# Kernel optimization log

Measured on AMD Instinct MI355X. Metric: run time of the kernel, lower is better.

The kernel has to match this reference:

```python
import jax, jax.numpy as jnp
import numpy as np

N = 50000      # nodes
E = 600000     # edges
D_IN = 128
D_HID = 128
D_OUT = 64
BN_EPS = 1e-5


def _linear(key, fan_in, fan_out):
    s = 1.0 / np.sqrt(fan_in)
    kw, kb = jax.random.split(key)
    W = jax.random.uniform(kw, (fan_in, fan_out), jnp.float32, -s, s)
    b = jax.random.uniform(kb, (fan_out,), jnp.float32, -s, s)
    return W, b


def setup_inputs() -> dict:
    key = jax.random.key(0)
    ks = jax.random.split(key, 6)
    x = jax.random.normal(ks[0], (N, D_IN), jnp.float32)
    edge_index = jax.random.randint(ks[1], (2, E), 0, N, dtype=jnp.int64)
    W1, b1 = _linear(ks[2], D_IN, D_HID)
    W2, b2 = _linear(ks[3], D_HID, D_HID)
    W3, b3 = _linear(ks[4], D_HID, D_OUT)
    g1 = jnp.ones((D_HID,), jnp.float32); be1 = jnp.zeros((D_HID,), jnp.float32)
    g2 = jnp.ones((D_HID,), jnp.float32); be2 = jnp.zeros((D_HID,), jnp.float32)
    return {"x": x, "edge_index": edge_index,
            "W1": W1, "b1": b1, "g1": g1, "be1": be1,
            "W2": W2, "b2": b2, "g2": g2, "be2": be2,
            "W3": W3, "b3": b3}


def _gin_conv(x, src, dst, W, b):
    # GIN aggregation: h_i = (1+eps)*x_i + sum_{j->i} x_j, eps=0, then linear
    agg = jax.ops.segment_sum(x[src], dst, num_segments=N)  # [N, d]
    return (agg + x) @ W + b


def _bn(x, gamma, beta):
    # BatchNorm1d in training mode: batch statistics over nodes
    m = x.mean(axis=0)
    v = x.var(axis=0)
    return (x - m) * jax.lax.rsqrt(v + BN_EPS) * gamma + beta


def reference(x, edge_index, W1, b1, g1, be1, W2, b2, g2, be2, W3, b3):
    src, dst = edge_index[0], edge_index[1]
    h = jax.nn.relu(_bn(_gin_conv(x, src, dst, W1, b1), g1, be1))
    h = jax.nn.relu(_bn(_gin_conv(h, src, dst, W2, b2), g2, be2))
    h = _gin_conv(h, src, dst, W3, b3)
    return jax.nn.log_softmax(h, axis=-1)
```

## Files before the change

kernel.cpp:

```cpp
#include <hip/hip_runtime.h>

#define BN_EPS 1e-5f

typedef __attribute__((ext_vector_type(8))) __bf16 bf16x8;
typedef __attribute__((ext_vector_type(4))) float f32x4;

__device__ __forceinline__ unsigned short f2bf(float f) {
    unsigned int u = __float_as_uint(f);
    u = (u + 0x7fffu + ((u >> 16) & 1u)) >> 16;
    return (unsigned short)u;
}
__device__ __forceinline__ float bfLo(unsigned int w) { return __uint_as_float(w << 16); }
__device__ __forceinline__ float bfHi(unsigned int w) { return __uint_as_float(w & 0xffff0000u); }

__device__ __forceinline__ void accRow(float* acc, uint4 v) {
    acc[0] += bfLo(v.x); acc[1] += bfHi(v.x);
    acc[2] += bfLo(v.y); acc[3] += bfHi(v.y);
    acc[4] += bfLo(v.z); acc[5] += bfHi(v.z);
    acc[6] += bfLo(v.w); acc[7] += bfHi(v.w);
}
__device__ __forceinline__ void accRowBN(float* acc, uint4 v, const float* a8, const float* c8) {
    acc[0] += fmaxf(fmaf(bfLo(v.x), a8[0], c8[0]), 0.f);
    acc[1] += fmaxf(fmaf(bfHi(v.x), a8[1], c8[1]), 0.f);
    acc[2] += fmaxf(fmaf(bfLo(v.y), a8[2], c8[2]), 0.f);
    acc[3] += fmaxf(fmaf(bfHi(v.y), a8[3], c8[3]), 0.f);
    acc[4] += fmaxf(fmaf(bfLo(v.z), a8[4], c8[4]), 0.f);
    acc[5] += fmaxf(fmaf(bfHi(v.z), a8[5], c8[5]), 0.f);
    acc[6] += fmaxf(fmaf(bfLo(v.w), a8[6], c8[6]), 0.f);
    acc[7] += fmaxf(fmaf(bfHi(v.w), a8[7], c8[7]), 0.f);
}


__global__ void hist_kernel(const int* __restrict__ dst, int* __restrict__ deg, int E) {
    int e = blockIdx.x * blockDim.x + threadIdx.x;
    if (e < E) atomicAdd(&deg[dst[e]], 1);
}

__global__ void scan_block(const int* __restrict__ deg, int* __restrict__ incl,
                           int* __restrict__ bsum, int N) {
    __shared__ int s[256];
    int i = blockIdx.x * 256 + threadIdx.x;
    int v = (i < N) ? deg[i] : 0;
    s[threadIdx.x] = v;
    __syncthreads();
#pragma unroll
    for (int off = 1; off < 256; off <<= 1) {
        int t = (threadIdx.x >= off) ? s[threadIdx.x - off] : 0;
        __syncthreads();
        s[threadIdx.x] += t;
        __syncthreads();
    }
    if (i < N) incl[i] = s[threadIdx.x];
    if (threadIdx.x == 255) bsum[blockIdx.x] = s[255];
}

__global__ void scan_top(int* __restrict__ bsum, int nb) {
    __shared__ int s[256];
    int v = (threadIdx.x < nb) ? bsum[threadIdx.x] : 0;
    s[threadIdx.x] = v;
    __syncthreads();
#pragma unroll
    for (int off = 1; off < 256; off <<= 1) {
        int t = (threadIdx.x >= off) ? s[threadIdx.x - off] : 0;
        __syncthreads();
        s[threadIdx.x] += t;
        __syncthreads();
    }
    if (threadIdx.x < nb) bsum[threadIdx.x] = s[threadIdx.x] - v;
}

__global__ void finalize_rowptr(const int* __restrict__ deg, const int* __restrict__ incl,
                                const int* __restrict__ boff, int* __restrict__ rowptr,
                                int* __restrict__ pos, int N, int E) {
    int i = blockIdx.x * 256 + threadIdx.x;
    if (i < N) {
        int r = incl[i] - deg[i] + boff[i >> 8];
        rowptr[i] = r;
        pos[i] = r;
    }
    if (i == 0) rowptr[N] = E;
}

__global__ void fill_kernel(const int* __restrict__ src, const int* __restrict__ dst,
                            int* __restrict__ pos, int* __restrict__ col, int E) {
    int e = blockIdx.x * blockDim.x + threadIdx.x;
    if (e < E) {
        int slot = atomicAdd(&pos[dst[e]], 1);
        col[slot] = src[e];
    }
}

__global__ void convert_and_prep(const float* __restrict__ x, unsigned short* __restrict__ hb,
                                 int total4,
                                 const float* __restrict__ W1, const float* __restrict__ W2,
                                 const float* __restrict__ W3,
                                 unsigned short* __restrict__ w1s, unsigned short* __restrict__ w2s,
                                 unsigned short* __restrict__ w3s) {
    int tid0 = blockIdx.x * blockDim.x + threadIdx.x;
    if (tid0 < 40960) {
        int idx = tid0;
        const float* W; unsigned short* O; int NOUT;
        if (idx < 16384)      { W = W1; O = w1s; NOUT = 128; }
        else if (idx < 32768) { W = W2; O = w2s; NOUT = 128; idx -= 16384; }
        else                  { W = W3; O = w3s; NOUT = 64;  idx -= 32768; }
        int j = idx & 7;
        int l = (idx >> 3) & 63;
        int q = (idx >> 9) & 3;
        int ct = idx >> 11;
        int k = q * 32 + ((l >> 4) & 3) * 8 + j;
        int c = ct * 16 + (l & 15);
        O[idx] = f2bf(W[(size_t)k * NOUT + c]);
    }
    int stride = gridDim.x * blockDim.x;
    for (int i = tid0; i < total4; i += stride) {
        float4 v = reinterpret_cast<const float4*>(x)[i];
        ushort4 o;
        o.x = f2bf(v.x); o.y = f2bf(v.y); o.z = f2bf(v.z); o.w = f2bf(v.w);
        reinterpret_cast<ushort4*>(hb)[i] = o;
    }
}

__global__ void gather_agg_bf(const unsigned short* __restrict__ h,
                              const int* __restrict__ rowptr, const int* __restrict__ col,
                              unsigned short* __restrict__ agg, int N) {
    int t = blockIdx.x * blockDim.x + threadIdx.x;
    int node = t >> 4;
    if (node >= N) return;
    int part = (t & 15) * 8;
    const unsigned short* hp = h + part;
    const int beg = rowptr[node], end = rowptr[node + 1];

    float acc[8];
    {
        uint4 sv = *reinterpret_cast<const uint4*>(hp + (size_t)node * 128);
        acc[0] = bfLo(sv.x); acc[1] = bfHi(sv.x);
        acc[2] = bfLo(sv.y); acc[3] = bfHi(sv.y);
        acc[4] = bfLo(sv.z); acc[5] = bfHi(sv.z);
        acc[6] = bfLo(sv.w); acc[7] = bfHi(sv.w);
    }
    int e = beg;
    for (; e + 3 < end; e += 4) {
        int s0 = col[e], s1 = col[e + 1], s2 = col[e + 2], s3 = col[e + 3];
        uint4 v0 = *reinterpret_cast<const uint4*>(hp + (size_t)s0 * 128);
        uint4 v1 = *reinterpret_cast<const uint4*>(hp + (size_t)s1 * 128);
        uint4 v2 = *reinterpret_cast<const uint4*>(hp + (size_t)s2 * 128);
        uint4 v3 = *reinterpret_cast<const uint4*>(hp + (size_t)s3 * 128);
        accRow(acc, v0); accRow(acc, v1); accRow(acc, v2); accRow(acc, v3);
    }
    for (; e < end; ++e)
        accRow(acc, *reinterpret_cast<const uint4*>(hp + (size_t)col[e] * 128));

    uint4 o;
    o.x = (unsigned int)f2bf(acc[0]) | ((unsigned int)f2bf(acc[1]) << 16);
    o.y = (unsigned int)f2bf(acc[2]) | ((unsigned int)f2bf(acc[3]) << 16);
    o.z = (unsigned int)f2bf(acc[4]) | ((unsigned int)f2bf(acc[5]) << 16);
    o.w = (unsigned int)f2bf(acc[6]) | ((unsigned int)f2bf(acc[7]) << 16);
    *reinterpret_cast<uint4*>(agg + (size_t)node * 128 + part) = o;
}

__global__ void gather_bn_agg(const unsigned short* __restrict__ raw,
                              const float* __restrict__ sumsPad, const float* __restrict__ sqsPad,
                              const float* __restrict__ g, const float* __restrict__ be,
                              const int* __restrict__ rowptr, const int* __restrict__ col,
                              unsigned short* __restrict__ agg, int N, float invN) {
    int t = blockIdx.x * blockDim.x + threadIdx.x;
    int node = t >> 4;
    if (node >= N) return;
    int part = (t & 15) * 8;
    const unsigned short* rp = raw + part;
    float a8[8], c8[8];
#pragma unroll
    for (int k = 0; k < 8; ++k) {
        int c = part + k;
        float m = sumsPad[c * 16] * invN;
        float v = sqsPad[c * 16] * invN - m * m;
        float ai = g[c] * rsqrtf(v + BN_EPS);
        a8[k] = ai;
        c8[k] = be[c] - m * ai;
    }
    const int beg = rowptr[node], end = rowptr[node + 1];
    float acc[8] = {0.f, 0.f, 0.f, 0.f, 0.f, 0.f, 0.f, 0.f};
    accRowBN(acc, *reinterpret_cast<const uint4*>(rp + (size_t)node * 128), a8, c8);
    int e = beg;
    for (; e + 3 < end; e += 4) {
        int s0 = col[e], s1 = col[e + 1], s2 = col[e + 2], s3 = col[e + 3];
        uint4 v0 = *reinterpret_cast<const uint4*>(rp + (size_t)s0 * 128);
        uint4 v1 = *reinterpret_cast<const uint4*>(rp + (size_t)s1 * 128);
        uint4 v2 = *reinterpret_cast<const uint4*>(rp + (size_t)s2 * 128);
        uint4 v3 = *reinterpret_cast<const uint4*>(rp + (size_t)s3 * 128);
        accRowBN(acc, v0, a8, c8); accRowBN(acc, v1, a8, c8);
        accRowBN(acc, v2, a8, c8); accRowBN(acc, v3, a8, c8);
    }
    for (; e < end; ++e)
        accRowBN(acc, *reinterpret_cast<const uint4*>(rp + (size_t)col[e] * 128), a8, c8);

    uint4 o;
    o.x = (unsigned int)f2bf(acc[0]) | ((unsigned int)f2bf(acc[1]) << 16);
    o.y = (unsigned int)f2bf(acc[2]) | ((unsigned int)f2bf(acc[3]) << 16);
    o.z = (unsigned int)f2bf(acc[4]) | ((unsigned int)f2bf(acc[5]) << 16);
    o.w = (unsigned int)f2bf(acc[6]) | ((unsigned int)f2bf(acc[7]) << 16);
    *reinterpret_cast<uint4*>(agg + (size_t)node * 128 + part) = o;
}

__global__ __launch_bounds__(256) void gemm128_stats(const unsigned short* __restrict__ A,
                                                     const unsigned short* __restrict__ Wsw,
                                                     const float* __restrict__ bias,
                                                     unsigned short* __restrict__ outb,
                                                     float* __restrict__ sumsPad,
                                                     float* __restrict__ sqsPad, int N) {
    __shared__ float red[2][4][128];
    const int lane = threadIdx.x & 63;
    const int w = threadIdx.x >> 6;
    const int r0 = blockIdx.x * 64 + w * 16;
    int arow = r0 + (lane & 15);
    if (arow >= N) arow = N - 1;
    const int kb = lane >> 4;
    const unsigned short* ap = A + (size_t)arow * 128 + kb * 8;

    bf16x8 a[4];
#pragma unroll
    for (int q = 0; q < 4; ++q) a[q] = *reinterpret_cast<const bf16x8*>(ap + q * 32);

    f32x4 acc[8];
#pragma unroll
    for (int ct = 0; ct < 8; ++ct) acc[ct] = (f32x4){0.f, 0.f, 0.f, 0.f};

    const bf16x8* wp = reinterpret_cast<const bf16x8*>(Wsw) + lane;
#pragma unroll
    for (int ct = 0; ct < 8; ++ct)
#pragma unroll
        for (int q = 0; q < 4; ++q)
            acc[ct] = __builtin_amdgcn_mfma_f32_16x16x32_bf16(a[q], wp[(ct * 4 + q) * 64],
                                                              acc[ct], 0, 0, 0);

    const int crow0 = r0 + (lane >> 4) * 4;
    const int ccol = lane & 15;
#pragma unroll
    for (int ct = 0; ct < 8; ++ct) {
        int c = ct * 16 + ccol;
        float bv = bias[c];
        float s = 0.f, qq = 0.f;
#pragma unroll
        for (int j = 0; j < 4; ++j) {
            int r = crow0 + j;
            if (r < N) {
                float o = acc[ct][j] + bv;
                outb[(size_t)r * 128 + c] = f2bf(o);
                s += o; qq += o * o;
            }
        }
        s += __shfl_xor(s, 16); s += __shfl_xor(s, 32);
        qq += __shfl_xor(qq, 16); qq += __shfl_xor(qq, 32);
        if (lane < 16) { red[0][w][c] = s; red[1][w][c] = qq; }
    }
    __syncthreads();
    int tid = threadIdx.x;
    if (tid < 128) {
        float S = red[0][0][tid] + red[0][1][tid] + red[0][2][tid] + red[0][3][tid];
        atomicAdd(&sumsPad[tid * 16], S);
    } else {
        int c = tid - 128;
        float Q = red[1][0][c] + red[1][1][c] + red[1][2][c] + red[1][3][c];
        atomicAdd(&sqsPad[c * 16], Q);
    }
}

__global__ __launch_bounds__(256) void gemm64_bn(const unsigned short* __restrict__ raw,
                                                 const float* __restrict__ sumsPad,
                                                 const float* __restrict__ sqsPad,
                                                 const float* __restrict__ g,
                                                 const float* __restrict__ be,
                                                 const unsigned short* __restrict__ Wsw,
                                                 unsigned short* __restrict__ M, int N,
                                                 float invN) {
    const int lane = threadIdx.x & 63;
    const int w = threadIdx.x >> 6;
    const int r0 = blockIdx.x * 64 + w * 16;
    int arow = r0 + (lane & 15);
    if (arow >= N) arow = N - 1;
    const int kb = lane >> 4;
    const unsigned short* ap = raw + (size_t)arow * 128 + kb * 8;

    bf16x8 a[4];
#pragma unroll
    for (int q = 0; q < 4; ++q) {
        uint4 rv = *reinterpret_cast<const uint4*>(ap + q * 32);
        float e0 = bfLo(rv.x), e1 = bfHi(rv.x), e2 = bfLo(rv.y), e3 = bfHi(rv.y);
        float e4 = bfLo(rv.z), e5 = bfHi(rv.z), e6 = bfLo(rv.w), e7 = bfHi(rv.w);
        float hh[8] = {e0, e1, e2, e3, e4, e5, e6, e7};
        uint4 hp;
        unsigned int pk[4];
#pragma unroll
        for (int p = 0; p < 4; ++p) {
            unsigned int lohi[2];
#pragma unroll
            for (int hl = 0; hl < 2; ++hl) {
                int j = p * 2 + hl;
                int c = q * 32 + kb * 8 + j;
                float mcol = sumsPad[c * 16] * invN;
                float var = sqsPad[c * 16] * invN - mcol * mcol;
                float ai = g[c] * rsqrtf(var + BN_EPS);
                float ci = be[c] - mcol * ai;
                lohi[hl] = f2bf(fmaxf(fmaf(hh[j], ai, ci), 0.f));
            }
            pk[p] = lohi[0] | (lohi[1] << 16);
        }
        hp.x = pk[0]; hp.y = pk[1]; hp.z = pk[2]; hp.w = pk[3];
        a[q] = *reinterpret_cast<bf16x8*>(&hp);
    }

    f32x4 acc[4];
#pragma unroll
    for (int ct = 0; ct < 4; ++ct) acc[ct] = (f32x4){0.f, 0.f, 0.f, 0.f};

    const bf16x8* wp = reinterpret_cast<const bf16x8*>(Wsw) + lane;
#pragma unroll
    for (int ct = 0; ct < 4; ++ct)
#pragma unroll
        for (int q = 0; q < 4; ++q)
            acc[ct] = __builtin_amdgcn_mfma_f32_16x16x32_bf16(a[q], wp[(ct * 4 + q) * 64],
                                                              acc[ct], 0, 0, 0);

    const int crow0 = r0 + (lane >> 4) * 4;
    const int ccol = lane & 15;
#pragma unroll
    for (int ct = 0; ct < 4; ++ct) {
        int c = ct * 16 + ccol;
#pragma unroll
        for (int j = 0; j < 4; ++j) {
            int r = crow0 + j;
            if (r < N) M[(size_t)r * 64 + c] = f2bf(acc[ct][j]);
        }
    }
}

__global__ void gather64_lsm(const unsigned short* __restrict__ M,
                             const int* __restrict__ rowptr, const int* __restrict__ col,
                             const float* __restrict__ bias, float* __restrict__ out, int N) {
    int t = blockIdx.x * blockDim.x + threadIdx.x;
    int node = t >> 3;
    if (node >= N) return;
    int part = (t & 7) * 8;
    const unsigned short* mp = M + part;
    const int beg = rowptr[node], end = rowptr[node + 1];

    float acc[8];
    {
        uint4 sv = *reinterpret_cast<const uint4*>(mp + (size_t)node * 64);
        acc[0] = bfLo(sv.x); acc[1] = bfHi(sv.x);
        acc[2] = bfLo(sv.y); acc[3] = bfHi(sv.y);
        acc[4] = bfLo(sv.z); acc[5] = bfHi(sv.z);
        acc[6] = bfLo(sv.w); acc[7] = bfHi(sv.w);
    }
    int e = beg;
    for (; e + 3 < end; e += 4) {
        int s0 = col[e], s1 = col[e + 1], s2 = col[e + 2], s3 = col[e + 3];
        uint4 v0 = *reinterpret_cast<const uint4*>(mp + (size_t)s0 * 64);
        uint4 v1 = *reinterpret_cast<const uint4*>(mp + (size_t)s1 * 64);
        uint4 v2 = *reinterpret_cast<const uint4*>(mp + (size_t)s2 * 64);
        uint4 v3 = *reinterpret_cast<const uint4*>(mp + (size_t)s3 * 64);
        accRow(acc, v0); accRow(acc, v1); accRow(acc, v2); accRow(acc, v3);
    }
    for (; e < end; ++e)
        accRow(acc, *reinterpret_cast<const uint4*>(mp + (size_t)col[e] * 64));

#pragma unroll
    for (int k = 0; k < 8; ++k) acc[k] += bias[part + k];

    float m = acc[0];
#pragma unroll
    for (int k = 1; k < 8; ++k) m = fmaxf(m, acc[k]);
#pragma unroll
    for (int off = 1; off < 8; off <<= 1) m = fmaxf(m, __shfl_xor(m, off));
    float s = 0.f;
#pragma unroll
    for (int k = 0; k < 8; ++k) s += __expf(acc[k] - m);
#pragma unroll
    for (int off = 1; off < 8; off <<= 1) s += __shfl_xor(s, off);
    float ml = m + __logf(s);

    float4 o0, o1;
    o0.x = acc[0] - ml; o0.y = acc[1] - ml; o0.z = acc[2] - ml; o0.w = acc[3] - ml;
    o1.x = acc[4] - ml; o1.y = acc[5] - ml; o1.z = acc[6] - ml; o1.w = acc[7] - ml;
    float* op = out + (size_t)node * 64 + part;
    *reinterpret_cast<float4*>(op) = o0;
    *reinterpret_cast<float4*>(op + 4) = o1;
}

extern "C" void kernel_launch(void* const* d_in, const int* in_sizes, int n_in,
                              void* d_out, int out_size, void* d_ws, size_t ws_size,
                              hipStream_t stream) {
    const float* x   = (const float*)d_in[0];
    const int*   ei  = (const int*)d_in[1];
    const float* W1  = (const float*)d_in[2];
    const float* b1  = (const float*)d_in[3];
    const float* g1  = (const float*)d_in[4];
    const float* be1 = (const float*)d_in[5];
    const float* W2  = (const float*)d_in[6];
    const float* b2  = (const float*)d_in[7];
    const float* g2  = (const float*)d_in[8];
    const float* be2 = (const float*)d_in[9];
    const float* W3  = (const float*)d_in[10];
    const float* b3  = (const float*)d_in[11];

    const int N = in_sizes[0] / 128;
    const int E = in_sizes[1] / 2;
    const int* src = ei;
    const int* dst = ei + E;

    float* statsPad = (float*)d_ws;
    float* sums1 = statsPad;
    float* sqs1  = statsPad + 2048;
    float* sums2 = statsPad + 4096;
    float* sqs2  = statsPad + 6144;
    int* deg    = (int*)(statsPad + 8192);
    int* pos    = deg + N;
    int* rowptr = pos + N;
    int* bsum   = rowptr + N + 1;
    int* colidx = bsum + 256;
    unsigned short* hb   = (unsigned short*)(colidx + E);
    unsigned short* rawb = hb + (size_t)N * 128;
    unsigned short* agb  = rawb + (size_t)N * 128;
    unsigned short* m3   = agb + (size_t)N * 128;
    unsigned short* w1s  = m3 + (size_t)N * 64;
    unsigned short* w2s  = w1s + 16384;
    unsigned short* w3s  = w2s + 16384;

    const int nChunks = (N + 255) / 256;
    const int eBlocks = (E + 255) / 256;
    const int gemmBlocks = (N + 63) / 64;
    const int gatherBlocks = (N * 16 + 255) / 256;
    const int gather64Blocks = (N * 8 + 255) / 256;
    const int total4 = N * 128 / 4;
    const float invN = 1.0f / N;

    hipMemsetAsync(statsPad, 0, 8192 * sizeof(float) + (size_t)N * sizeof(int), stream);

    convert_and_prep<<<2048, 256, 0, stream>>>(x, hb, total4, W1, W2, W3, w1s, w2s, w3s);
    hist_kernel<<<eBlocks, 256, 0, stream>>>(dst, deg, E);
    scan_block<<<nChunks, 256, 0, stream>>>(deg, pos, bsum, N);
    scan_top<<<1, 256, 0, stream>>>(bsum, nChunks);
    finalize_rowptr<<<nChunks, 256, 0, stream>>>(deg, pos, bsum, rowptr, pos, N, E);
    fill_kernel<<<eBlocks, 256, 0, stream>>>(src, dst, pos, colidx, E);

    gather_agg_bf<<<gatherBlocks, 256, 0, stream>>>(hb, rowptr, colidx, agb, N);
    gemm128_stats<<<gemmBlocks, 256, 0, stream>>>(agb, w1s, b1, rawb, sums1, sqs1, N);

    gather_bn_agg<<<gatherBlocks, 256, 0, stream>>>(rawb, sums1, sqs1, g1, be1, rowptr, colidx,
                                                    agb, N, invN);
    gemm128_stats<<<gemmBlocks, 256, 0, stream>>>(agb, w2s, b2, rawb, sums2, sqs2, N);

    gemm64_bn<<<gemmBlocks, 256, 0, stream>>>(rawb, sums2, sqs2, g2, be2, w3s, m3, N, invN);
    gather64_lsm<<<gather64Blocks, 256, 0, stream>>>(m3, rowptr, colidx, b3, (float*)d_out, N);
}
```

Baseline: 252.5 us.

## Fuse neighbor gather into GEMM kernels and merge rowptr scan into one kernel

The separate gather kernels are folded into the MFMA GEMM kernels: each lane gathers and sums its row's neighbor features in registers, then feeds the bf16 result straight to the MFMAs. This removes writing and re-reading the intermediate aggregate buffer. The last block of each GEMM now computes the BatchNorm scale and shift once, so later kernels no longer recompute them per element. The three scan kernels become one kernel that uses an atomic spin barrier, which depends on all blocks being resident at once. Gather parallelism drops from 16 to 4 threads per node, with more loads in flight per thread.

Result: slower. 398.4 us (+57.8%).

```diff
diff --git a/kernel.cpp b/kernel.cpp
--- a/kernel.cpp
+++ b/kernel.cpp
@@ -13,81 +13,21 @@
 __device__ __forceinline__ float bfLo(unsigned int w) { return __uint_as_float(w << 16); }
 __device__ __forceinline__ float bfHi(unsigned int w) { return __uint_as_float(w & 0xffff0000u); }
 
-__device__ __forceinline__ void accRow(float* acc, uint4 v) {
+__device__ __forceinline__ void acc8_raw(float* acc, uint4 v) {
     acc[0] += bfLo(v.x); acc[1] += bfHi(v.x);
     acc[2] += bfLo(v.y); acc[3] += bfHi(v.y);
     acc[4] += bfLo(v.z); acc[5] += bfHi(v.z);
     acc[6] += bfLo(v.w); acc[7] += bfHi(v.w);
 }
-__device__ __forceinline__ void accRowBN(float* acc, uint4 v, const float* a8, const float* c8) {
-    acc[0] += fmaxf(fmaf(bfLo(v.x), a8[0], c8[0]), 0.f);
-    acc[1] += fmaxf(fmaf(bfHi(v.x), a8[1], c8[1]), 0.f);
-    acc[2] += fmaxf(fmaf(bfLo(v.y), a8[2], c8[2]), 0.f);
-    acc[3] += fmaxf(fmaf(bfHi(v.y), a8[3], c8[3]), 0.f);
-    acc[4] += fmaxf(fmaf(bfLo(v.z), a8[4], c8[4]), 0.f);
-    acc[5] += fmaxf(fmaf(bfHi(v.z), a8[5], c8[5]), 0.f);
-    acc[6] += fmaxf(fmaf(bfLo(v.w), a8[6], c8[6]), 0.f);
-    acc[7] += fmaxf(fmaf(bfHi(v.w), a8[7], c8[7]), 0.f);
-}
-
-
-__global__ void hist_kernel(const int* __restrict__ dst, int* __restrict__ deg, int E) {
-    int e = blockIdx.x * blockDim.x + threadIdx.x;
-    if (e < E) atomicAdd(&deg[dst[e]], 1);
-}
-
-__global__ void scan_block(const int* __restrict__ deg, int* __restrict__ incl,
-                           int* __restrict__ bsum, int N) {
-    __shared__ int s[256];
-    int i = blockIdx.x * 256 + threadIdx.x;
-    int v = (i < N) ? deg[i] : 0;
-    s[threadIdx.x] = v;
-    __syncthreads();
-#pragma unroll
-    for (int off = 1; off < 256; off <<= 1) {
-        int t = (threadIdx.x >= off) ? s[threadIdx.x - off] : 0;
-        __syncthreads();
-        s[threadIdx.x] += t;
-        __syncthreads();
-    }
-    if (i < N) incl[i] = s[threadIdx.x];
-    if (threadIdx.x == 255) bsum[blockIdx.x] = s[255];
-}
-
-__global__ void scan_top(int* __restrict__ bsum, int nb) {
-    __shared__ int s[256];
-    int v = (threadIdx.x < nb) ? bsum[threadIdx.x] : 0;
-    s[threadIdx.x] = v;
-    __syncthreads();
-#pragma unroll
-    for (int off = 1; off < 256; off <<= 1) {
-        int t = (threadIdx.x >= off) ? s[threadIdx.x - off] : 0;
-        __syncthreads();
-        s[threadIdx.x] += t;
-        __syncthreads();
-    }
-    if (threadIdx.x < nb) bsum[threadIdx.x] = s[threadIdx.x] - v;
-}
-
-__global__ void finalize_rowptr(const int* __restrict__ deg, const int* __restrict__ incl,
-                                const int* __restrict__ boff, int* __restrict__ rowptr,
-                                int* __restrict__ pos, int N, int E) {
-    int i = blockIdx.x * 256 + threadIdx.x;
-    if (i < N) {
-        int r = incl[i] - deg[i] + boff[i >> 8];
-        rowptr[i] = r;
-        pos[i] = r;
-    }
-    if (i == 0) rowptr[N] = E;
-}
-
-__global__ void fill_kernel(const int* __restrict__ src, const int* __restrict__ dst,
-                            int* __restrict__ pos, int* __restrict__ col, int E) {
-    int e = blockIdx.x * blockDim.x + threadIdx.x;
-    if (e < E) {
-        int slot = atomicAdd(&pos[dst[e]], 1);
-        col[slot] = src[e];
-    }
+__device__ __forceinline__ void acc8_bn(float* acc, uint4 v, const float* a, const float* c) {
+    acc[0] += fmaxf(fmaf(bfLo(v.x), a[0], c[0]), 0.f);
+    acc[1] += fmaxf(fmaf(bfHi(v.x), a[1], c[1]), 0.f);
+    acc[2] += fmaxf(fmaf(bfLo(v.y), a[2], c[2]), 0.f);
+    acc[3] += fmaxf(fmaf(bfHi(v.y), a[3], c[3]), 0.f);
+    acc[4] += fmaxf(fmaf(bfLo(v.z), a[4], c[4]), 0.f);
+    acc[5] += fmaxf(fmaf(bfHi(v.z), a[5], c[5]), 0.f);
+    acc[6] += fmaxf(fmaf(bfLo(v.w), a[6], c[6]), 0.f);
+    acc[7] += fmaxf(fmaf(bfHi(v.w), a[7], c[7]), 0.f);
 }
 
 __global__ void convert_and_prep(const float* __restrict__ x, unsigned short* __restrict__ hb,
@@ -120,118 +60,159 @@
     }
 }
 
-__global__ void gather_agg_bf(const unsigned short* __restrict__ h,
-                              const int* __restrict__ rowptr, const int* __restrict__ col,
-                              unsigned short* __restrict__ agg, int N) {
-    int t = blockIdx.x * blockDim.x + threadIdx.x;
-    int node = t >> 4;
-    if (node >= N) return;
-    int part = (t & 15) * 8;
-    const unsigned short* hp = h + part;
-    const int beg = rowptr[node], end = rowptr[node + 1];
-
-    float acc[8];
-    {
-        uint4 sv = *reinterpret_cast<const uint4*>(hp + (size_t)node * 128);
-        acc[0] = bfLo(sv.x); acc[1] = bfHi(sv.x);
-        acc[2] = bfLo(sv.y); acc[3] = bfHi(sv.y);
-        acc[4] = bfLo(sv.z); acc[5] = bfHi(sv.z);
-        acc[6] = bfLo(sv.w); acc[7] = bfHi(sv.w);
-    }
-    int e = beg;
-    for (; e + 3 < end; e += 4) {
-        int s0 = col[e], s1 = col[e + 1], s2 = col[e + 2], s3 = col[e + 3];
-        uint4 v0 = *reinterpret_cast<const uint4*>(hp + (size_t)s0 * 128);
-        uint4 v1 = *reinterpret_cast<const uint4*>(hp + (size_t)s1 * 128);
-        uint4 v2 = *reinterpret_cast<const uint4*>(hp + (size_t)s2 * 128);
-        uint4 v3 = *reinterpret_cast<const uint4*>(hp + (size_t)s3 * 128);
-        accRow(acc, v0); accRow(acc, v1); accRow(acc, v2); accRow(acc, v3);
-    }
-    for (; e < end; ++e)
-        accRow(acc, *reinterpret_cast<const uint4*>(hp + (size_t)col[e] * 128));
-
-    uint4 o;
-    o.x = (unsigned int)f2bf(acc[0]) | ((unsigned int)f2bf(acc[1]) << 16);
-    o.y = (unsigned int)f2bf(acc[2]) | ((unsigned int)f2bf(acc[3]) << 16);
-    o.z = (unsigned int)f2bf(acc[4]) | ((unsigned int)f2bf(acc[5]) << 16);
-    o.w = (unsigned int)f2bf(acc[6]) | ((unsigned int)f2bf(acc[7]) << 16);
-    *reinterpret_cast<uint4*>(agg + (size_t)node * 128 + part) = o;
-}
-
-__global__ void gather_bn_agg(const unsigned short* __restrict__ raw,
-                              const float* __restrict__ sumsPad, const float* __restrict__ sqsPad,
-                              const float* __restrict__ g, const float* __restrict__ be,
-                              const int* __restrict__ rowptr, const int* __restrict__ col,
-                              unsigned short* __restrict__ agg, int N, float invN) {
-    int t = blockIdx.x * blockDim.x + threadIdx.x;
-    int node = t >> 4;
-    if (node >= N) return;
-    int part = (t & 15) * 8;
-    const unsigned short* rp = raw + part;
-    float a8[8], c8[8];
-#pragma unroll
-    for (int k = 0; k < 8; ++k) {
-        int c = part + k;
-        float m = sumsPad[c * 16] * invN;
-        float v = sqsPad[c * 16] * invN - m * m;
-        float ai = g[c] * rsqrtf(v + BN_EPS);
-        a8[k] = ai;
-        c8[k] = be[c] - m * ai;
-    }
-    const int beg = rowptr[node], end = rowptr[node + 1];
-    float acc[8] = {0.f, 0.f, 0.f, 0.f, 0.f, 0.f, 0.f, 0.f};
-    accRowBN(acc, *reinterpret_cast<const uint4*>(rp + (size_t)node * 128), a8, c8);
-    int e = beg;
-    for (; e + 3 < end; e += 4) {
-        int s0 = col[e], s1 = col[e + 1], s2 = col[e + 2], s3 = col[e + 3];
-        uint4 v0 = *reinterpret_cast<const uint4*>(rp + (size_t)s0 * 128);
-        uint4 v1 = *reinterpret_cast<const uint4*>(rp + (size_t)s1 * 128);
-        uint4 v2 = *reinterpret_cast<const uint4*>(rp + (size_t)s2 * 128);
-        uint4 v3 = *reinterpret_cast<const uint4*>(rp + (size_t)s3 * 128);
-        accRowBN(acc, v0, a8, c8); accRowBN(acc, v1, a8, c8);
-        accRowBN(acc, v2, a8, c8); accRowBN(acc, v3, a8, c8);
-    }
-    for (; e < end; ++e)
-        accRowBN(acc, *reinterpret_cast<const uint4*>(rp + (size_t)col[e] * 128), a8, c8);
-
-    uint4 o;
-    o.x = (unsigned int)f2bf(acc[0]) | ((unsigned int)f2bf(acc[1]) << 16);
-    o.y = (unsigned int)f2bf(acc[2]) | ((unsigned int)f2bf(acc[3]) << 16);
-    o.z = (unsigned int)f2bf(acc[4]) | ((unsigned int)f2bf(acc[5]) << 16);
-    o.w = (unsigned int)f2bf(acc[6]) | ((unsigned int)f2bf(acc[7]) << 16);
-    *reinterpret_cast<uint4*>(agg + (size_t)node * 128 + part) = o;
-}
-
-__global__ __launch_bounds__(256) void gemm128_stats(const unsigned short* __restrict__ A,
-                                                     const unsigned short* __restrict__ Wsw,
-                                                     const float* __restrict__ bias,
-                                                     unsigned short* __restrict__ outb,
-                                                     float* __restrict__ sumsPad,
-                                                     float* __restrict__ sqsPad, int N) {
+
+__global__ void hist_kernel(const int* __restrict__ dst, int* __restrict__ deg, int E) {
+    int e = blockIdx.x * blockDim.x + threadIdx.x;
+    if (e < E) atomicAdd(&deg[dst[e]], 1);
+}
+
+__global__ void build_rowptr(const int* __restrict__ deg, int* __restrict__ rowptr,
+                             int* __restrict__ pos, int* __restrict__ bsum,
+                             int* __restrict__ arrive, int N, int E, int nChunks) {
+    __shared__ int s[256];
+    const int tid = threadIdx.x;
+    const int b = blockIdx.x;
+    const int i = b * 256 + tid;
+    const int v = (i < N) ? deg[i] : 0;
+    s[tid] = v;
+    __syncthreads();
+#pragma unroll
+    for (int off = 1; off < 256; off <<= 1) {
+        int t = (tid >= off) ? s[tid - off] : 0;
+        __syncthreads();
+        s[tid] += t;
+        __syncthreads();
+    }
+    const int incl = s[tid];
+    if (tid == 255) bsum[b] = incl;
+    __threadfence();
+    __syncthreads();
+    if (tid == 0) {
+        __hip_atomic_fetch_add(arrive, 1, __ATOMIC_ACQ_REL, __HIP_MEMORY_SCOPE_AGENT);
+        while (__hip_atomic_load(arrive, __ATOMIC_ACQUIRE, __HIP_MEMORY_SCOPE_AGENT) < nChunks) {}
+    }
+    __syncthreads();
+    int val = (tid < b && tid < nChunks)
+                  ? __hip_atomic_load(&bsum[tid], __ATOMIC_RELAXED, __HIP_MEMORY_SCOPE_AGENT)
+                  : 0;
+    __syncthreads();
+    s[tid] = val;
+    __syncthreads();
+#pragma unroll
+    for (int off = 128; off > 0; off >>= 1) {
+        if (tid < off) s[tid] += s[tid + off];
+        __syncthreads();
+    }
+    const int base = s[0];
+    if (i < N) {
+        int r = incl - v + base;
+        rowptr[i] = r;
+        pos[i] = r;
+    }
+    if (b == 0 && tid == 0) rowptr[N] = E;
+}
+
+__global__ void fill_kernel(const int* __restrict__ src, const int* __restrict__ dst,
+                            int* __restrict__ pos, int* __restrict__ col, int E) {
+    int e = blockIdx.x * blockDim.x + threadIdx.x;
+    if (e < E) {
+        int slot = atomicAdd(&pos[dst[e]], 1);
+        col[slot] = src[e];
+    }
+}
+
+template <bool HAS_BN>
+__global__ __launch_bounds__(256) void fused_g_gemm128(
+    const unsigned short* __restrict__ h, const int* __restrict__ rowptr,
+    const int* __restrict__ col, const float* __restrict__ aC, const float* __restrict__ cC,
+    const unsigned short* __restrict__ Wsw, const float* __restrict__ bias,
+    unsigned short* __restrict__ outb, float* __restrict__ sumsPad, float* __restrict__ sqsPad,
+    int* __restrict__ doneCnt, const float* __restrict__ gOwn, const float* __restrict__ beOwn,
+    float* __restrict__ aOut, float* __restrict__ cOut, int N, float invN) {
     __shared__ float red[2][4][128];
+    __shared__ int lastFlag;
     const int lane = threadIdx.x & 63;
     const int w = threadIdx.x >> 6;
     const int r0 = blockIdx.x * 64 + w * 16;
-    int arow = r0 + (lane & 15);
-    if (arow >= N) arow = N - 1;
+    int row = r0 + (lane & 15);
+    if (row >= N) row = N - 1;
     const int kb = lane >> 4;
-    const unsigned short* ap = A + (size_t)arow * 128 + kb * 8;
+    const int cbase = kb * 8;
+
+    float a4[4][8], c4[4][8];
+    if (HAS_BN) {
+#pragma unroll
+        for (int q = 0; q < 4; ++q) {
+            const float4* ap = reinterpret_cast<const float4*>(aC + q * 32 + cbase);
+            const float4* cp = reinterpret_cast<const float4*>(cC + q * 32 + cbase);
+            float4 A0 = ap[0], A1 = ap[1], C0 = cp[0], C1 = cp[1];
+            a4[q][0] = A0.x; a4[q][1] = A0.y; a4[q][2] = A0.z; a4[q][3] = A0.w;
+            a4[q][4] = A1.x; a4[q][5] = A1.y; a4[q][6] = A1.z; a4[q][7] = A1.w;
+            c4[q][0] = C0.x; c4[q][1] = C0.y; c4[q][2] = C0.z; c4[q][3] = C0.w;
+            c4[q][4] = C1.x; c4[q][5] = C1.y; c4[q][6] = C1.z; c4[q][7] = C1.w;
+        }
+    }
+
+    float acc[4][8];
+    {
+        const unsigned short* sp = h + (size_t)row * 128 + cbase;
+#pragma unroll
+        for (int q = 0; q < 4; ++q) {
+            uint4 v = *reinterpret_cast<const uint4*>(sp + q * 32);
+#pragma unroll
+            for (int j = 0; j < 8; ++j) acc[q][j] = 0.f;
+            if (HAS_BN) acc8_bn(acc[q], v, a4[q], c4[q]);
+            else        acc8_raw(acc[q], v);
+        }
+    }
+    const int beg = rowptr[row], end = rowptr[row + 1];
+    int e = beg;
+    for (; e + 1 < end; e += 2) {
+        int s0 = col[e], s1 = col[e + 1];
+        const unsigned short* p0 = h + (size_t)s0 * 128 + cbase;
+        const unsigned short* p1 = h + (size_t)s1 * 128 + cbase;
+        uint4 v0[4], v1[4];
+#pragma unroll
+        for (int q = 0; q < 4; ++q) v0[q] = *reinterpret_cast<const uint4*>(p0 + q * 32);
+#pragma unroll
+        for (int q = 0; q < 4; ++q) v1[q] = *reinterpret_cast<const uint4*>(p1 + q * 32);
+#pragma unroll
+        for (int q = 0; q < 4; ++q) {
+            if (HAS_BN) { acc8_bn(acc[q], v0[q], a4[q], c4[q]); acc8_bn(acc[q], v1[q], a4[q], c4[q]); }
+            else        { acc8_raw(acc[q], v0[q]); acc8_raw(acc[q], v1[q]); }
+        }
+    }
+    if (e < end) {
+        const unsigned short* p0 = h + (size_t)col[e] * 128 + cbase;
+#pragma unroll
+        for (int q = 0; q < 4; ++q) {
+            uint4 v = *reinterpret_cast<const uint4*>(p0 + q * 32);
+            if (HAS_BN) acc8_bn(acc[q], v, a4[q], c4[q]);
+            else        acc8_raw(acc[q], v);
+        }
+    }
 
     bf16x8 a[4];
 #pragma unroll
-    for (int q = 0; q < 4; ++q) a[q] = *reinterpret_cast<const bf16x8*>(ap + q * 32);
-
-    f32x4 acc[8];
-#pragma unroll
-    for (int ct = 0; ct < 8; ++ct) acc[ct] = (f32x4){0.f, 0.f, 0.f, 0.f};
-
+    for (int q = 0; q < 4; ++q) {
+        uint4 hp;
+        hp.x = (unsigned int)f2bf(acc[q][0]) | ((unsigned int)f2bf(acc[q][1]) << 16);
+        hp.y = (unsigned int)f2bf(acc[q][2]) | ((unsigned int)f2bf(acc[q][3]) << 16);
+        hp.z = (unsigned int)f2bf(acc[q][4]) | ((unsigned int)f2bf(acc[q][5]) << 16);
+        hp.w = (unsigned int)f2bf(acc[q][6]) | ((unsigned int)f2bf(acc[q][7]) << 16);
+        a[q] = *reinterpret_cast<bf16x8*>(&hp);
+    }
+
+    f32x4 mac[8];
+#pragma unroll
+    for (int ct = 0; ct < 8; ++ct) mac[ct] = (f32x4){0.f, 0.f, 0.f, 0.f};
     const bf16x8* wp = reinterpret_cast<const bf16x8*>(Wsw) + lane;
 #pragma unroll
     for (int ct = 0; ct < 8; ++ct)
 #pragma unroll
         for (int q = 0; q < 4; ++q)
-            acc[ct] = __builtin_amdgcn_mfma_f32_16x16x32_bf16(a[q], wp[(ct * 4 + q) * 64],
-                                                              acc[ct], 0, 0, 0);
+            mac[ct] = __builtin_amdgcn_mfma_f32_16x16x32_bf16(a[q], wp[(ct * 4 + q) * 64],
+                                                              mac[ct], 0, 0, 0);
 
     const int crow0 = r0 + (lane >> 4) * 4;
     const int ccol = lane & 15;
@@ -244,7 +225,7 @@
         for (int j = 0; j < 4; ++j) {
             int r = crow0 + j;
             if (r < N) {
-                float o = acc[ct][j] + bv;
+                float o = mac[ct][j] + bv;
                 outb[(size_t)r * 128 + c] = f2bf(o);
                 s += o; qq += o * o;
             }
@@ -263,16 +244,25 @@
         float Q = red[1][0][c] + red[1][1][c] + red[1][2][c] + red[1][3][c];
         atomicAdd(&sqsPad[c * 16], Q);
     }
+    __threadfence();
+    if (tid == 0) lastFlag = (atomicAdd(doneCnt, 1) == (int)gridDim.x - 1);
+    __syncthreads();
+    if (lastFlag && tid < 128) {
+        float S = __hip_atomic_load(&sumsPad[tid * 16], __ATOMIC_RELAXED, __HIP_MEMORY_SCOPE_AGENT);
+        float Q = __hip_atomic_load(&sqsPad[tid * 16], __ATOMIC_RELAXED, __HIP_MEMORY_SCOPE_AGENT);
+        float m = S * invN;
+        float var = Q * invN - m * m;
+        float ai = gOwn[tid] * rsqrtf(var + BN_EPS);
+        aOut[tid] = ai;
+        cOut[tid] = beOwn[tid] - m * ai;
+    }
 }
 
 __global__ __launch_bounds__(256) void gemm64_bn(const unsigned short* __restrict__ raw,
-                                                 const float* __restrict__ sumsPad,
-                                                 const float* __restrict__ sqsPad,
-                                                 const float* __restrict__ g,
-                                                 const float* __restrict__ be,
+                                                 const float* __restrict__ aC,
+                                                 const float* __restrict__ cC,
                                                  const unsigned short* __restrict__ Wsw,
-                                                 unsigned short* __restrict__ M, int N,
-                                                 float invN) {
+                                                 unsigned short* __restrict__ M, int N) {
     const int lane = threadIdx.x & 63;
     const int w = threadIdx.x >> 6;
     const int r0 = blockIdx.x * 64 + w * 16;
@@ -285,34 +275,24 @@
 #pragma unroll
     for (int q = 0; q < 4; ++q) {
         uint4 rv = *reinterpret_cast<const uint4*>(ap + q * 32);
-        float e0 = bfLo(rv.x), e1 = bfHi(rv.x), e2 = bfLo(rv.y), e3 = bfHi(rv.y);
-        float e4 = bfLo(rv.z), e5 = bfHi(rv.z), e6 = bfLo(rv.w), e7 = bfHi(rv.w);
-        float hh[8] = {e0, e1, e2, e3, e4, e5, e6, e7};
+        const float4* af = reinterpret_cast<const float4*>(aC + q * 32 + kb * 8);
+        const float4* cf = reinterpret_cast<const float4*>(cC + q * 32 + kb * 8);
+        float4 A0 = af[0], A1 = af[1], C0 = cf[0], C1 = cf[1];
         uint4 hp;
-        unsigned int pk[4];
-#pragma unroll
-        for (int p = 0; p < 4; ++p) {
-            unsigned int lohi[2];
-#pragma unroll
-            for (int hl = 0; hl < 2; ++hl) {
-                int j = p * 2 + hl;
-                int c = q * 32 + kb * 8 + j;
-                float mcol = sumsPad[c * 16] * invN;
-                float var = sqsPad[c * 16] * invN - mcol * mcol;
-                float ai = g[c] * rsqrtf(var + BN_EPS);
-                float ci = be[c] - mcol * ai;
-                lohi[hl] = f2bf(fmaxf(fmaf(hh[j], ai, ci), 0.f));
-            }
-            pk[p] = lohi[0] | (lohi[1] << 16);
-        }
-        hp.x = pk[0]; hp.y = pk[1]; hp.z = pk[2]; hp.w = pk[3];
+        hp.x = (unsigned int)f2bf(fmaxf(fmaf(bfLo(rv.x), A0.x, C0.x), 0.f)) |
+               ((unsigned int)f2bf(fmaxf(fmaf(bfHi(rv.x), A0.y, C0.y), 0.f)) << 16);
+        hp.y = (unsigned int)f2bf(fmaxf(fmaf(bfLo(rv.y), A0.z, C0.z), 0.f)) |
+               ((unsigned int)f2bf(fmaxf(fmaf(bfHi(rv.y), A0.w, C0.w), 0.f)) << 16);
+        hp.z = (unsigned int)f2bf(fmaxf(fmaf(bfLo(rv.z), A1.x, C1.x), 0.f)) |
+               ((unsigned int)f2bf(fmaxf(fmaf(bfHi(rv.z), A1.y, C1.y), 0.f)) << 16);
+        hp.w = (unsigned int)f2bf(fmaxf(fmaf(bfLo(rv.w), A1.z, C1.z), 0.f)) |
+               ((unsigned int)f2bf(fmaxf(fmaf(bfHi(rv.w), A1.w, C1.w), 0.f)) << 16);
         a[q] = *reinterpret_cast<bf16x8*>(&hp);
     }
 
     f32x4 acc[4];
 #pragma unroll
     for (int ct = 0; ct < 4; ++ct) acc[ct] = (f32x4){0.f, 0.f, 0.f, 0.f};
-
     const bf16x8* wp = reinterpret_cast<const bf16x8*>(Wsw) + lane;
 #pragma unroll
     for (int ct = 0; ct < 4; ++ct)
@@ -359,10 +339,10 @@
         uint4 v1 = *reinterpret_cast<const uint4*>(mp + (size_t)s1 * 64);
         uint4 v2 = *reinterpret_cast<const uint4*>(mp + (size_t)s2 * 64);
         uint4 v3 = *reinterpret_cast<const uint4*>(mp + (size_t)s3 * 64);
-        accRow(acc, v0); accRow(acc, v1); accRow(acc, v2); accRow(acc, v3);
+        acc8_raw(acc, v0); acc8_raw(acc, v1); acc8_raw(acc, v2); acc8_raw(acc, v3);
     }
     for (; e < end; ++e)
-        accRow(acc, *reinterpret_cast<const uint4*>(mp + (size_t)col[e] * 64));
+        acc8_raw(acc, *reinterpret_cast<const uint4*>(mp + (size_t)col[e] * 64));
 
 #pragma unroll
     for (int k = 0; k < 8; ++k) acc[k] += bias[part + k];
@@ -413,15 +393,20 @@
     float* sqs1  = statsPad + 2048;
     float* sums2 = statsPad + 4096;
     float* sqs2  = statsPad + 6144;
-    int* deg    = (int*)(statsPad + 8192);
+    float* a1    = statsPad + 8192;
+    float* c1    = a1 + 128;
+    float* a2    = c1 + 128;
+    float* c2    = a2 + 128;
+    int* cnts   = (int*)(c2 + 128);
+    int* deg    = cnts + 64;
     int* pos    = deg + N;
     int* rowptr = pos + N;
     int* bsum   = rowptr + N + 1;
     int* colidx = bsum + 256;
     unsigned short* hb   = (unsigned short*)(colidx + E);
-    unsigned short* rawb = hb + (size_t)N * 128;
-    unsigned short* agb  = rawb + (size_t)N * 128;
-    unsigned short* m3   = agb + (size_t)N * 128;
+    unsigned short* raw1 = hb + (size_t)N * 128;
+    unsigned short* raw2 = raw1 + (size_t)N * 128;
+    unsigned short* m3   = raw2 + (size_t)N * 128;
     unsigned short* w1s  = m3 + (size_t)N * 64;
     unsigned short* w2s  = w1s + 16384;
     unsigned short* w3s  = w2s + 16384;
@@ -429,27 +414,26 @@
     const int nChunks = (N + 255) / 256;
     const int eBlocks = (E + 255) / 256;
     const int gemmBlocks = (N + 63) / 64;
-    const int gatherBlocks = (N * 16 + 255) / 256;
     const int gather64Blocks = (N * 8 + 255) / 256;
     const int total4 = N * 128 / 4;
     const float invN = 1.0f / N;
 
-    hipMemsetAsync(statsPad, 0, 8192 * sizeof(float) + (size_t)N * sizeof(int), stream);
+    const size_t zeroBytes = (8192 + 512) * sizeof(float) + (64 + (size_t)N) * sizeof(int);
+    hipMemsetAsync(statsPad, 0, zeroBytes, stream);
 
     convert_and_prep<<<2048, 256, 0, stream>>>(x, hb, total4, W1, W2, W3, w1s, w2s, w3s);
     hist_kernel<<<eBlocks, 256, 0, stream>>>(dst, deg, E);
-    scan_block<<<nChunks, 256, 0, stream>>>(deg, pos, bsum, N);
-    scan_top<<<1, 256, 0, stream>>>(bsum, nChunks);
-    finalize_rowptr<<<nChunks, 256, 0, stream>>>(deg, pos, bsum, rowptr, pos, N, E);
+    build_rowptr<<<nChunks, 256, 0, stream>>>(deg, rowptr, pos, bsum, cnts + 2, N, E, nChunks);
     fill_kernel<<<eBlocks, 256, 0, stream>>>(src, dst, pos, colidx, E);
 
-    gather_agg_bf<<<gatherBlocks, 256, 0, stream>>>(hb, rowptr, colidx, agb, N);
-    gemm128_stats<<<gemmBlocks, 256, 0, stream>>>(agb, w1s, b1, rawb, sums1, sqs1, N);
-
-    gather_bn_agg<<<gatherBlocks, 256, 0, stream>>>(rawb, sums1, sqs1, g1, be1, rowptr, colidx,
-                                                    agb, N, invN);
-    gemm128_stats<<<gemmBlocks, 256, 0, stream>>>(agb, w2s, b2, rawb, sums2, sqs2, N);
-
-    gemm64_bn<<<gemmBlocks, 256, 0, stream>>>(rawb, sums2, sqs2, g2, be2, w3s, m3, N, invN);
+    fused_g_gemm128<false><<<gemmBlocks, 256, 0, stream>>>(
+        hb, rowptr, colidx, nullptr, nullptr, w1s, b1, raw1, sums1, sqs1,
+        cnts + 0, g1, be1, a1, c1, N, invN);
+
+    fused_g_gemm128<true><<<gemmBlocks, 256, 0, stream>>>(
+        raw1, rowptr, colidx, a1, c1, w2s, b2, raw2, sums2, sqs2,
+        cnts + 1, g2, be2, a2, c2, N, invN);
+
+    gemm64_bn<<<gemmBlocks, 256, 0, stream>>>(raw2, a2, c2, w3s, m3, N);
     gather64_lsm<<<gather64Blocks, 256, 0, stream>>>(m3, rowptr, colidx, b3, (float*)d_out, N);
 }
```

## Fuse CSR construction into fewer launches using grid-wide spin barriers

Applied to the files above, without the earlier changes.

Folds the degree histogram into the input-conversion kernel and replaces the separate scan_block, scan_top, finalize_rowptr and fill kernels with a single build_csr kernel. That kernel uses atomic-counter grid barriers so block offsets and the edge fill happen within one launch. The aim is to cut kernel launch overhead and the serial gaps between small kernels. The cost is a persistent-style barrier that relies on all 196 blocks being co-resident, and a fill loop limited to nChunks*256 threads.

New measurement: 282.3 us. 1.12x slower.

```diff
diff --git a/kernel.cpp b/kernel.cpp
--- a/kernel.cpp
+++ b/kernel.cpp
@@ -30,73 +30,15 @@
     acc[7] += fmaxf(fmaf(bfHi(v.w), a8[7], c8[7]), 0.f);
 }
 
-
-__global__ void hist_kernel(const int* __restrict__ dst, int* __restrict__ deg, int E) {
-    int e = blockIdx.x * blockDim.x + threadIdx.x;
-    if (e < E) atomicAdd(&deg[dst[e]], 1);
-}
-
-__global__ void scan_block(const int* __restrict__ deg, int* __restrict__ incl,
-                           int* __restrict__ bsum, int N) {
-    __shared__ int s[256];
-    int i = blockIdx.x * 256 + threadIdx.x;
-    int v = (i < N) ? deg[i] : 0;
-    s[threadIdx.x] = v;
-    __syncthreads();
-#pragma unroll
-    for (int off = 1; off < 256; off <<= 1) {
-        int t = (threadIdx.x >= off) ? s[threadIdx.x - off] : 0;
-        __syncthreads();
-        s[threadIdx.x] += t;
-        __syncthreads();
-    }
-    if (i < N) incl[i] = s[threadIdx.x];
-    if (threadIdx.x == 255) bsum[blockIdx.x] = s[255];
-}
-
-__global__ void scan_top(int* __restrict__ bsum, int nb) {
-    __shared__ int s[256];
-    int v = (threadIdx.x < nb) ? bsum[threadIdx.x] : 0;
-    s[threadIdx.x] = v;
-    __syncthreads();
-#pragma unroll
-    for (int off = 1; off < 256; off <<= 1) {
-        int t = (threadIdx.x >= off) ? s[threadIdx.x - off] : 0;
-        __syncthreads();
-        s[threadIdx.x] += t;
-        __syncthreads();
-    }
-    if (threadIdx.x < nb) bsum[threadIdx.x] = s[threadIdx.x] - v;
-}
-
-__global__ void finalize_rowptr(const int* __restrict__ deg, const int* __restrict__ incl,
-                                const int* __restrict__ boff, int* __restrict__ rowptr,
-                                int* __restrict__ pos, int N, int E) {
-    int i = blockIdx.x * 256 + threadIdx.x;
-    if (i < N) {
-        int r = incl[i] - deg[i] + boff[i >> 8];
-        rowptr[i] = r;
-        pos[i] = r;
-    }
-    if (i == 0) rowptr[N] = E;
-}
-
-__global__ void fill_kernel(const int* __restrict__ src, const int* __restrict__ dst,
-                            int* __restrict__ pos, int* __restrict__ col, int E) {
-    int e = blockIdx.x * blockDim.x + threadIdx.x;
-    if (e < E) {
-        int slot = atomicAdd(&pos[dst[e]], 1);
-        col[slot] = src[e];
-    }
-}
-
-__global__ void convert_and_prep(const float* __restrict__ x, unsigned short* __restrict__ hb,
-                                 int total4,
-                                 const float* __restrict__ W1, const float* __restrict__ W2,
-                                 const float* __restrict__ W3,
-                                 unsigned short* __restrict__ w1s, unsigned short* __restrict__ w2s,
-                                 unsigned short* __restrict__ w3s) {
+__global__ void convert_prep_hist(const float* __restrict__ x, unsigned short* __restrict__ hb,
+                                  int total4,
+                                  const float* __restrict__ W1, const float* __restrict__ W2,
+                                  const float* __restrict__ W3,
+                                  unsigned short* __restrict__ w1s, unsigned short* __restrict__ w2s,
+                                  unsigned short* __restrict__ w3s,
+                                  const int* __restrict__ dst, int* __restrict__ deg, int E) {
     int tid0 = blockIdx.x * blockDim.x + threadIdx.x;
+    int stride = gridDim.x * blockDim.x;
     if (tid0 < 40960) {
         int idx = tid0;
         const float* W; unsigned short* O; int NOUT;
@@ -111,12 +53,71 @@
         int c = ct * 16 + (l & 15);
         O[idx] = f2bf(W[(size_t)k * NOUT + c]);
     }
-    int stride = gridDim.x * blockDim.x;
     for (int i = tid0; i < total4; i += stride) {
         float4 v = reinterpret_cast<const float4*>(x)[i];
         ushort4 o;
         o.x = f2bf(v.x); o.y = f2bf(v.y); o.z = f2bf(v.z); o.w = f2bf(v.w);
         reinterpret_cast<ushort4*>(hb)[i] = o;
+    }
+    for (int e = tid0; e < E; e += stride) atomicAdd(&deg[dst[e]], 1);
+}
+
+__global__ void build_csr(const int* __restrict__ deg, int* __restrict__ rowptr,
+                          int* __restrict__ pos, int* __restrict__ bsum,
+                          int* __restrict__ cnt,
+                          const int* __restrict__ src, const int* __restrict__ dst,
+                          int* __restrict__ col, int N, int E, int nChunks) {
+    __shared__ int s[256];
+    const int tid = threadIdx.x;
+    const int b = blockIdx.x;
+    const int i = b * 256 + tid;
+    const int v = (i < N) ? deg[i] : 0;
+    s[tid] = v;
+    __syncthreads();
+#pragma unroll
+    for (int off = 1; off < 256; off <<= 1) {
+        int t = (tid >= off) ? s[tid - off] : 0;
+        __syncthreads();
+        s[tid] += t;
+        __syncthreads();
+    }
+    const int incl = s[tid];
+    if (tid == 255) bsum[b] = incl;
+    __threadfence();
+    __syncthreads();
+    if (tid == 0) {
+        __hip_atomic_fetch_add(&cnt[0], 1, __ATOMIC_ACQ_REL, __HIP_MEMORY_SCOPE_AGENT);
+        while (__hip_atomic_load(&cnt[0], __ATOMIC_ACQUIRE, __HIP_MEMORY_SCOPE_AGENT) < nChunks) {}
+    }
+    __syncthreads();
+    int val = (tid < b)
+                  ? __hip_atomic_load(&bsum[tid], __ATOMIC_RELAXED, __HIP_MEMORY_SCOPE_AGENT)
+                  : 0;
+    s[tid] = val;
+    __syncthreads();
+#pragma unroll
+    for (int off = 128; off > 0; off >>= 1) {
+        if (tid < off) s[tid] += s[tid + off];
+        __syncthreads();
+    }
+    const int base = s[0];
+    if (i < N) {
+        int r = incl - v + base;
+        rowptr[i] = r;
+        pos[i] = r;
+    }
+    if (b == 0 && tid == 0) rowptr[N] = E;
+    __threadfence();
+    __syncthreads();
+    if (tid == 0) {
+        __hip_atomic_fetch_add(&cnt[1], 1, __ATOMIC_ACQ_REL, __HIP_MEMORY_SCOPE_AGENT);
+        while (__hip_atomic_load(&cnt[1], __ATOMIC_ACQUIRE, __HIP_MEMORY_SCOPE_AGENT) < nChunks) {}
+    }
+    __syncthreads();
+    const int gstride = nChunks * 256;
+    for (int e = b * 256 + tid; e < E; e += gstride) {
+        int slot = atomicAdd(&pos[dst[e]], 1);
+        col[slot] = src[e];
     }
 }
 
@@ -285,10 +286,8 @@
 #pragma unroll
     for (int q = 0; q < 4; ++q) {
         uint4 rv = *reinterpret_cast<const uint4*>(ap + q * 32);
-        float e0 = bfLo(rv.x), e1 = bfHi(rv.x), e2 = bfLo(rv.y), e3 = bfHi(rv.y);
-        float e4 = bfLo(rv.z), e5 = bfHi(rv.z), e6 = bfLo(rv.w), e7 = bfHi(rv.w);
-        float hh[8] = {e0, e1, e2, e3, e4, e5, e6, e7};
-        uint4 hp;
+        float hh[8] = {bfLo(rv.x), bfHi(rv.x), bfLo(rv.y), bfHi(rv.y),
+                       bfLo(rv.z), bfHi(rv.z), bfLo(rv.w), bfHi(rv.w)};
         unsigned int pk[4];
 #pragma unroll
         for (int p = 0; p < 4; ++p) {
@@ -305,6 +304,7 @@
             }
             pk[p] = lohi[0] | (lohi[1] << 16);
         }
+        uint4 hp;
         hp.x = pk[0]; hp.y = pk[1]; hp.z = pk[2]; hp.w = pk[3];
         a[q] = *reinterpret_cast<bf16x8*>(&hp);
     }
@@ -413,7 +413,8 @@
     float* sqs1  = statsPad + 2048;
     float* sums2 = statsPad + 4096;
     float* sqs2  = statsPad + 6144;
-    int* deg    = (int*)(statsPad + 8192);
+    int* cnts   = (int*)(statsPad + 8192);
+    int* deg    = cnts + 64;
     int* pos    = deg + N;
     int* rowptr = pos + N;
     int* bsum   = rowptr + N + 1;
@@ -433,15 +434,14 @@
     const int gather64Blocks = (N * 8 + 255) / 256;
     const int total4 = N * 128 / 4;
     const float invN = 1.0f / N;
-
-    hipMemsetAsync(statsPad, 0, 8192 * sizeof(float) + (size_t)N * sizeof(int), stream);
-
-    convert_and_prep<<<2048, 256, 0, stream>>>(x, hb, total4, W1, W2, W3, w1s, w2s, w3s);
-    hist_kernel<<<eBlocks, 256, 0, stream>>>(dst, deg, E);
-    scan_block<<<nChunks, 256, 0, stream>>>(deg, pos, bsum, N);
-    scan_top<<<1, 256, 0, stream>>>(bsum, nChunks);
-    finalize_rowptr<<<nChunks, 256, 0, stream>>>(deg, pos, bsum, rowptr, pos, N, E);
-    fill_kernel<<<eBlocks, 256, 0, stream>>>(src, dst, pos, colidx, E);
+    (void)eBlocks;
+
+    hipMemsetAsync(statsPad, 0, 8192 * sizeof(float) + (64 + (size_t)N) * sizeof(int), stream);
+
+    convert_prep_hist<<<2048, 256, 0, stream>>>(x, hb, total4, W1, W2, W3, w1s, w2s, w3s,
+                                                dst, deg, E);
+    build_csr<<<nChunks, 256, 0, stream>>>(deg, rowptr, pos, bsum, cnts, src, dst, colidx,
+                                           N, E, nChunks);
 
     gather_agg_bf<<<gatherBlocks, 256, 0, stream>>>(hb, rowptr, colidx, agb, N);
     gemm128_stats<<<gemmBlocks, 256, 0, stream>>>(agb, w1s, b1, rawb, sums1, sqs1, N);
```
